# Kernel tuning notes

Measured on AMD Instinct MI355X. Metric: run time of the kernel, lower is better.

Reference implementation:

```python
import jax, jax.numpy as jnp
import numpy as np

D_MODEL = 1024
NUM_HEADS = 16
HEAD_DIM = D_MODEL // NUM_HEADS
SCALE = HEAD_DIM ** -0.5


def setup_inputs() -> dict:
    key = jax.random.key(0)
    ks = jax.random.split(key, 9)
    s = 1.0 / np.sqrt(D_MODEL)
    return {
        "query": jax.random.normal(ks[0], (4, 2048, D_MODEL), dtype=jnp.float32),
        "Wq": jax.random.normal(ks[1], (D_MODEL, D_MODEL), dtype=jnp.float32) * s,
        "bq": jax.random.normal(ks[2], (D_MODEL,), dtype=jnp.float32) * 0.01,
        "Wk": jax.random.normal(ks[3], (D_MODEL, D_MODEL), dtype=jnp.float32) * s,
        "bk": jax.random.normal(ks[4], (D_MODEL,), dtype=jnp.float32) * 0.01,
        "Wv": jax.random.normal(ks[5], (D_MODEL, D_MODEL), dtype=jnp.float32) * s,
        "bv": jax.random.normal(ks[6], (D_MODEL,), dtype=jnp.float32) * 0.01,
        "Wo": jax.random.normal(ks[7], (D_MODEL, D_MODEL), dtype=jnp.float32) * s,
        "bo": jax.random.normal(ks[8], (D_MODEL,), dtype=jnp.float32) * 0.01,
    }


def reference(query, Wq, bq, Wk, bk, Wv, bv, Wo, bo):
    # Self-attention (key=value=query). dropout=0, no mask, so chunked
    # computation equals full softmax attention exactly.
    b, s, d = query.shape
    q = (query @ Wq + bq).reshape(b, s, NUM_HEADS, HEAD_DIM)
    k = (query @ Wk + bk).reshape(b, s, NUM_HEADS, HEAD_DIM)
    v = (query @ Wv + bv).reshape(b, s, NUM_HEADS, HEAD_DIM)
    # scores: [b, h, s_q, s_k]
    scores = jnp.einsum("bqhd,bkhd->bhqk", q, k) * SCALE
    attn = jax.nn.softmax(scores, axis=-1)
    ctx = jnp.einsum("bhqk,bkhd->bqhd", attn, v).reshape(b, s, d)
    return ctx @ Wo + bo
```

## Files before the change

kernel.cpp:

```cpp
#include <hip/hip_runtime.h>
#include <stdint.h>

#define NHEADS 16
#define HDIM   64
#define SEQ    2048
#define BATCH  4
#define DM     1024
#define MTOT   (BATCH*SEQ)
#define SCALE  0.125f
#define QSCALE 0.18033688011112042f

typedef unsigned short u16;
typedef __attribute__((ext_vector_type(8))) short short8;
typedef __attribute__((ext_vector_type(4))) float f32x4;
typedef __attribute__((ext_vector_type(16))) float f32x16;
typedef __attribute__((ext_vector_type(4))) unsigned int u32x4;

__device__ __forceinline__ u16 f2bf(float f) {
  uint32_t u = __builtin_bit_cast(uint32_t, f);
  u += 0x7FFFu + ((u >> 16) & 1u);
  return (u16)(u >> 16);
}

__device__ __forceinline__ f32x4 mfma16(short8 a, short8 b, f32x4 c) {
  return __builtin_amdgcn_mfma_f32_16x16x32_bf16(a, b, c, 0, 0, 0);
}
__device__ __forceinline__ f32x16 mfma32(short8 a, short8 b, f32x16 c) {
  return __builtin_amdgcn_mfma_f32_32x32x16_bf16(a, b, c, 0, 0, 0);
}

__device__ __forceinline__ void gload16(const u16* g, u16* l) {
  __builtin_amdgcn_global_load_lds((const __attribute__((address_space(1))) void*)g,
                                   (__attribute__((address_space(3))) void*)l,
                                   16, 0, 0);
}

#define LDSP(base, row, boff) \
  ((u16*)((char*)(base) + (((row) << 7) + ((boff) ^ (((row) & 7) << 4)))))

__global__ __launch_bounds__(256) void k_conv(const float* __restrict__ in, u16* __restrict__ out) {
  size_t i = (size_t)blockIdx.x * 256 + threadIdx.x;
  const float4* p = (const float4*)(in + i * 8);
  float4 a = p[0], b = p[1];
  u16 r[8] = {f2bf(a.x), f2bf(a.y), f2bf(a.z), f2bf(a.w),
              f2bf(b.x), f2bf(b.y), f2bf(b.z), f2bf(b.w)};
  *(short8*)(out + i * 8) = *(const short8*)r;
}

__global__ __launch_bounds__(256) void k_convw(const float* __restrict__ w0, const float* __restrict__ w1,
                                               const float* __restrict__ w2, const float* __restrict__ w3,
                                               u16* __restrict__ o0, u16* __restrict__ o1,
                                               u16* __restrict__ o2, u16* __restrict__ o3) {
  const float* W = blockIdx.z==0?w0: blockIdx.z==1?w1: blockIdx.z==2?w2:w3;
  u16* O        = blockIdx.z==0?o0: blockIdx.z==1?o1: blockIdx.z==2?o2:o3;
  __shared__ float tile[32][33];
  int t = threadIdx.x;
  int k0 = blockIdx.y*32, n0 = blockIdx.x*32;
  int r = t >> 5, c = t & 31;
  #pragma unroll
  for (int p = 0; p < 4; ++p) tile[r + 8*p][c] = W[(size_t)(k0 + r + 8*p)*DM + n0 + c];
  __syncthreads();
  #pragma unroll
  for (int p = 0; p < 4; ++p) O[(size_t)(n0 + r + 8*p)*DM + k0 + c] = f2bf(tile[c][r + 8*p]);
}

template<int MODE>
__global__ __launch_bounds__(256) void k_gemm(
    const u16* __restrict__ A,
    const u16* __restrict__ WtQ, const u16* __restrict__ WtK, const u16* __restrict__ WtV,
    const float* __restrict__ bQ, const float* __restrict__ bK, const float* __restrict__ bV,
    u16* __restrict__ oQ, u16* __restrict__ oK, u16* __restrict__ oV,
    float* __restrict__ oF)
{
  __shared__ u16 As[128*32];
  __shared__ u16 Bs[128*32];
  const int t = threadIdx.x;
  const int lane = t & 63;
  const int lo = lane & 15, q4 = lane >> 4;
  const int w  = t >> 6, wm = w >> 1, wn = w & 1;

  int m0, n0, z;
  if (MODE == 0) {
    int L = blockIdx.x + 8 * blockIdx.y + 512 * blockIdx.z;
    int work = (L & 7) * 192 + (L >> 3);
    z  = work % 3;
    n0 = ((work / 3) & 7) * 128;
    m0 = (work / 24) * 128;
  } else {
    int L = blockIdx.x + 8 * blockIdx.y;
    int work = (L & 7) * 64 + (L >> 3);
    z  = 0;
    n0 = (work & 7) * 128;
    m0 = (work >> 3) * 128;
  }

  const u16* Wt; const float* bias;
  if (MODE == 0) {
    Wt   = (z==0)?WtQ:(z==1)?WtK:WtV;
    bias = (z==0)?bQ:(z==1)?bK:bV;
  } else { Wt = WtQ; bias = bQ; }

  f32x4 acc[4][4] = {};

  const int gr = lane >> 2;
  const int gc = (lane & 3) * 8;

  for (int kt = 0; kt < 32; ++kt) {
    const int k0 = kt * 32;
    __syncthreads();
    gload16(A  + (size_t)(m0 + w*32 +  0 + gr)*DM + k0 + gc, As + (w*32 +  0)*32);
    gload16(A  + (size_t)(m0 + w*32 + 16 + gr)*DM + k0 + gc, As + (w*32 + 16)*32);
    gload16(Wt + (size_t)(n0 + w*32 +  0 + gr)*DM + k0 + gc, Bs + (w*32 +  0)*32);
    gload16(Wt + (size_t)(n0 + w*32 + 16 + gr)*DM + k0 + gc, Bs + (w*32 + 16)*32);
    __syncthreads();

    short8 af[4], bf[4];
    #pragma unroll
    for (int i = 0; i < 4; ++i)
      af[i] = *(const short8*)(As + (wm*64 + i*16 + lo)*32 + q4*8);
    #pragma unroll
    for (int i = 0; i < 4; ++i)
      bf[i] = *(const short8*)(Bs + (wn*64 + i*16 + lo)*32 + q4*8);
    #pragma unroll
    for (int i = 0; i < 4; ++i)
      #pragma unroll
      for (int j = 0; j < 4; ++j)
        acc[i][j] = mfma16(af[i], bf[j], acc[i][j]);
  }

  #pragma unroll
  for (int i = 0; i < 4; ++i) {
    #pragma unroll
    for (int j = 0; j < 4; ++j) {
      int col = n0 + wn*64 + j*16 + lo;
      float bvv = bias[col];
      #pragma unroll
      for (int r = 0; r < 4; ++r) {
        int row = m0 + wm*64 + i*16 + q4*4 + r;
        float v = acc[i][j][r] + bvv;
        if (MODE == 0) {
          int b = row >> 11, s = row & 2047, h = col >> 6, d = col & 63;
          if (z == 2) oV[(size_t)((b*16 + h)*64 + d)*SEQ + s] = f2bf(v);
          else if (z == 0) oQ[(size_t)((b*16 + h)*SEQ + s)*HDIM + d] = f2bf(v * QSCALE);
          else             oK[(size_t)((b*16 + h)*SEQ + s)*HDIM + d] = f2bf(v);
        } else {
          oF[(size_t)row*DM + col] = v;
        }
      }
    }
  }
}

__global__ __launch_bounds__(256, 2) void k_attn(
    const u16* __restrict__ Q,
    const u16* __restrict__ K,
    const u16* __restrict__ VT,
    u16* __restrict__ O)
{
  __shared__ u16 lds[16384];
  u16* Ks = lds;
  u16* Vs = lds + 4096;
  const int t = threadIdx.x, lane = t & 63, w = t >> 6;
  const int l31 = lane & 31, h = lane >> 5;
  const int bh = blockIdx.x, qt = blockIdx.y;
  const int qw = qt*256 + w*64;

  const u16* Qp = Q  + ((size_t)bh * SEQ + qw) * HDIM;
  const u16* Kp = K  + (size_t)bh * SEQ * HDIM;
  const u16* Vp = VT + (size_t)bh * HDIM * SEQ;

  short8 qf[2][4];
  #pragma unroll
  for (int g = 0; g < 2; ++g)
    #pragma unroll
    for (int c = 0; c < 4; ++c)
      qf[g][c] = *(const short8*)(Qp + (size_t)(g*32 + l31)*HDIM + c*16 + h*8);

  f32x16 acc[2][2] = {};
  float l_run[2] = {0.f, 0.f};

  const int sr = t >> 3, sc = t & 7;
  const u16* Kg = Kp + (size_t)sr * HDIM;
  const u16* Vg = Vp + (size_t)sr * SEQ;
  short8 kr0 = *(const short8*)(Kg + sc*8);
  short8 kr1 = *(const short8*)(Kg + (size_t)32*HDIM + sc*8);
  short8 vr0 = *(const short8*)(Vg + sc*8);
  short8 vr1 = *(const short8*)(Vg + (size_t)32*SEQ + sc*8);

  for (int kt = 0; kt < 32; ++kt) {
    __syncthreads();
    *(short8*)LDSP(Ks, sr,      sc*16) = kr0;
    *(short8*)LDSP(Ks, sr + 32, sc*16) = kr1;
    *(short8*)LDSP(Vs, sr,      sc*16) = vr0;
    *(short8*)LDSP(Vs, sr + 32, sc*16) = vr1;
    {
      int kn = (kt + 1 < 32 ? kt + 1 : 31) * 64;
      kr0 = *(const short8*)(Kg + (size_t)kn*HDIM + sc*8);
      kr1 = *(const short8*)(Kg + (size_t)(kn+32)*HDIM + sc*8);
      vr0 = *(const short8*)(Vg + kn + sc*8);
      vr1 = *(const short8*)(Vg + (size_t)32*SEQ + kn + sc*8);
    }
    __syncthreads();

    #pragma unroll
    for (int kb = 0; kb < 2; ++kb) {
      short8 kf[4];
      #pragma unroll
      for (int c = 0; c < 4; ++c)
        kf[c] = *(const short8*)LDSP(Ks, kb*32 + l31, c*32 + h*16);
      short8 vf[2][2];
      #pragma unroll
      for (int dt = 0; dt < 2; ++dt)
        #pragma unroll
        for (int k2 = 0; k2 < 2; ++k2)
          vf[dt][k2] = *(const short8*)LDSP(Vs, dt*32 + l31, kb*64 + k2*32 + h*16);

      #pragma unroll
      for (int g = 0; g < 2; ++g) {
        f32x16 s = {};
        #pragma unroll
        for (int c = 0; c < 4; ++c) s = mfma32(kf[c], qf[g][c], s);

        float sum = 0.f;
        uint32_t W[8];
        #pragma unroll
        for (int i8 = 0; i8 < 8; ++i8) {
          float pe = exp2f(s[2*i8]);
          float po = exp2f(s[2*i8+1]);
          sum += pe + po;
          W[i8] = __builtin_amdgcn_perm(__builtin_bit_cast(uint32_t, po),
                                        __builtin_bit_cast(uint32_t, pe),
                                        0x07060302u);
        }
        l_run[g] += sum;

        #pragma unroll
        for (int k2 = 0; k2 < 2; ++k2) {
          auto r0 = __builtin_amdgcn_permlane32_swap(W[4*k2 + 0], W[4*k2 + 2], false, false);
          auto r1 = __builtin_amdgcn_permlane32_swap(W[4*k2 + 1], W[4*k2 + 3], false, false);
          u32x4 pw; pw[0] = r0[0]; pw[1] = r1[0]; pw[2] = r0[1]; pw[3] = r1[1];
          short8 pf = __builtin_bit_cast(short8, pw);
          #pragma unroll
          for (int dt = 0; dt < 2; ++dt)
            acc[g][dt] = mfma32(vf[dt][k2], pf, acc[g][dt]);
        }
      }
    }
  }

  __syncthreads();
  u16* ep = lds + w*4096;
  #pragma unroll
  for (int g = 0; g < 2; ++g) {
    float lt = l_run[g] + __shfl_xor(l_run[g], 32);
    float inv = 1.f / lt;
    #pragma unroll
    for (int dt = 0; dt < 2; ++dt)
      #pragma unroll
      for (int i = 0; i < 16; ++i) {
        int d = dt*32 + (i & 3) + 8*(i >> 2) + 4*h;
        *LDSP(ep, g*32 + l31, 2*d) = f2bf(acc[g][dt][i] * inv);
      }
  }
  const int b = bh >> 4, hh = bh & 15;
  #pragma unroll
  for (int it = 0; it < 8; ++it) {
    int row = it*8 + (lane >> 3);
    int s = qw + row;
    short8 v = *(const short8*)LDSP(ep, row, (lane & 7)*16);
    *(short8*)(O + ((size_t)(b*SEQ + s)*NHEADS + hh)*HDIM + (lane & 7)*8) = v;
  }
}

extern "C" void kernel_launch(void* const* d_in, const int* in_sizes, int n_in,
                              void* d_out, int out_size, void* d_ws, size_t ws_size,
                              hipStream_t stream) {
  const float* query = (const float*)d_in[0];
  const float* Wq = (const float*)d_in[1]; const float* bq = (const float*)d_in[2];
  const float* Wk = (const float*)d_in[3]; const float* bk = (const float*)d_in[4];
  const float* Wv = (const float*)d_in[5]; const float* bv = (const float*)d_in[6];
  const float* Wo = (const float*)d_in[7]; const float* bo = (const float*)d_in[8];
  float* out = (float*)d_out;

  u16* qb  = (u16*)d_ws;
  u16* wt0 = qb  + (size_t)MTOT*DM;
  u16* wt1 = wt0 + (size_t)DM*DM;
  u16* wt2 = wt1 + (size_t)DM*DM;
  u16* wt3 = wt2 + (size_t)DM*DM;
  u16* qp  = wt3 + (size_t)DM*DM;
  u16* kp  = qp  + (size_t)MTOT*DM;
  u16* vt  = kp  + (size_t)MTOT*DM;

  k_conv<<<dim3(MTOT*DM/8/256), 256, 0, stream>>>(query, qb);
  k_convw<<<dim3(32, 32, 4), 256, 0, stream>>>(Wq, Wk, Wv, Wo, wt0, wt1, wt2, wt3);
  k_gemm<0><<<dim3(8, 64, 3), 256, 0, stream>>>(qb, wt0, wt1, wt2, bq, bk, bv, qp, kp, vt, nullptr);
  k_attn<<<dim3(64, 8), 256, 0, stream>>>(qp, kp, vt, qb );
  k_gemm<1><<<dim3(8, 64, 1), 256, 0, stream>>>(qb, wt3, nullptr, nullptr, bo, nullptr, nullptr,
                                                nullptr, nullptr, nullptr, out);
}
```

Before: 306.2 us.

## Restructure attention kernel: 8 waves of 32 rows, double-buffered K/V LDS

The attention kernel now launches 512 threads per block, each wave owning 32 query rows instead of 64. K/V tiles are double-buffered in LDS, with one barrier per iteration instead of two, so staging the next tile overlaps compute. It also uses a raw hardware exp2 and packed bf16 epilogue stores. The trade-off is more waves sharing each K/V tile, giving fewer MFMAs per LDS read, plus the approximate exp instruction's precision.

```diff
diff --git a/kernel.cpp b/kernel.cpp
--- a/kernel.cpp
+++ b/kernel.cpp
@@ -20,6 +20,14 @@
   uint32_t u = __builtin_bit_cast(uint32_t, f);
   u += 0x7FFFu + ((u >> 16) & 1u);
   return (u16)(u >> 16);
+}
+
+__device__ __forceinline__ float fexp2(float x) {
+#if __has_builtin(__builtin_amdgcn_exp2f)
+  return __builtin_amdgcn_exp2f(x);
+#else
+  float r; asm("v_exp_f32 %0, %1\n\ts_nop 1" : "=v"(r) : "v"(x)); return r;
+#endif
 }
 
 __device__ __forceinline__ f32x4 mfma16(short8 a, short8 b, f32x4 c) {
@@ -151,120 +159,114 @@
   }
 }
 
-__global__ __launch_bounds__(256, 2) void k_attn(
+__global__ __launch_bounds__(512, 4) void k_attn(
     const u16* __restrict__ Q,
     const u16* __restrict__ K,
     const u16* __restrict__ VT,
     u16* __restrict__ O)
 {
   __shared__ u16 lds[16384];
-  u16* Ks = lds;
-  u16* Vs = lds + 4096;
   const int t = threadIdx.x, lane = t & 63, w = t >> 6;
   const int l31 = lane & 31, h = lane >> 5;
   const int bh = blockIdx.x, qt = blockIdx.y;
-  const int qw = qt*256 + w*64;
+  const int qw = qt*256 + w*32;
 
   const u16* Qp = Q  + ((size_t)bh * SEQ + qw) * HDIM;
   const u16* Kp = K  + (size_t)bh * SEQ * HDIM;
   const u16* Vp = VT + (size_t)bh * HDIM * SEQ;
 
-  short8 qf[2][4];
-  #pragma unroll
-  for (int g = 0; g < 2; ++g)
-    #pragma unroll
-    for (int c = 0; c < 4; ++c)
-      qf[g][c] = *(const short8*)(Qp + (size_t)(g*32 + l31)*HDIM + c*16 + h*8);
-
-  f32x16 acc[2][2] = {};
-  float l_run[2] = {0.f, 0.f};
+  short8 qf[4];
+  #pragma unroll
+  for (int c = 0; c < 4; ++c)
+    qf[c] = *(const short8*)(Qp + (size_t)l31*HDIM + c*16 + h*8);
+
+  f32x16 acc[2] = {};
+  float l_run = 0.f;
 
   const int sr = t >> 3, sc = t & 7;
   const u16* Kg = Kp + (size_t)sr * HDIM;
   const u16* Vg = Vp + (size_t)sr * SEQ;
-  short8 kr0 = *(const short8*)(Kg + sc*8);
-  short8 kr1 = *(const short8*)(Kg + (size_t)32*HDIM + sc*8);
-  short8 vr0 = *(const short8*)(Vg + sc*8);
-  short8 vr1 = *(const short8*)(Vg + (size_t)32*SEQ + sc*8);
+
+  short8 kr = *(const short8*)(Kg + sc*8);
+  short8 vr = *(const short8*)(Vg + sc*8);
+  *(short8*)LDSP(lds,        sr, sc*16) = kr;
+  *(short8*)LDSP(lds + 4096, sr, sc*16) = vr;
+  kr = *(const short8*)(Kg + (size_t)64*HDIM + sc*8);
+  vr = *(const short8*)(Vg + 64 + sc*8);
+  __syncthreads();
 
   for (int kt = 0; kt < 32; ++kt) {
-    __syncthreads();
-    *(short8*)LDSP(Ks, sr,      sc*16) = kr0;
-    *(short8*)LDSP(Ks, sr + 32, sc*16) = kr1;
-    *(short8*)LDSP(Vs, sr,      sc*16) = vr0;
-    *(short8*)LDSP(Vs, sr + 32, sc*16) = vr1;
-    {
-      int kn = (kt + 1 < 32 ? kt + 1 : 31) * 64;
-      kr0 = *(const short8*)(Kg + (size_t)kn*HDIM + sc*8);
-      kr1 = *(const short8*)(Kg + (size_t)(kn+32)*HDIM + sc*8);
-      vr0 = *(const short8*)(Vg + kn + sc*8);
-      vr1 = *(const short8*)(Vg + (size_t)32*SEQ + kn + sc*8);
+    u16* Ksc = lds + (size_t)(kt & 1) * 8192;
+    u16* Vsc = Ksc + 4096;
+    if (kt + 1 < 32) {
+      u16* Ksn = lds + (size_t)((kt + 1) & 1) * 8192;
+      *(short8*)LDSP(Ksn,        sr, sc*16) = kr;
+      *(short8*)LDSP(Ksn + 4096, sr, sc*16) = vr;
+      int kn = (kt + 2 < 32 ? kt + 2 : 31) * 64;
+      kr = *(const short8*)(Kg + (size_t)kn*HDIM + sc*8);
+      vr = *(const short8*)(Vg + kn + sc*8);
     }
-    __syncthreads();
 
     #pragma unroll
     for (int kb = 0; kb < 2; ++kb) {
       short8 kf[4];
       #pragma unroll
       for (int c = 0; c < 4; ++c)
-        kf[c] = *(const short8*)LDSP(Ks, kb*32 + l31, c*32 + h*16);
-      short8 vf[2][2];
-      #pragma unroll
-      for (int dt = 0; dt < 2; ++dt)
+        kf[c] = *(const short8*)LDSP(Ksc, kb*32 + l31, c*32 + h*16);
+
+      f32x16 s = {};
+      #pragma unroll
+      for (int c = 0; c < 4; ++c) s = mfma32(kf[c], qf[c], s);
+
+      float sum = 0.f;
+      uint32_t W[8];
+      #pragma unroll
+      for (int i8 = 0; i8 < 8; ++i8) {
+        float pe = fexp2(s[2*i8]);
+        float po = fexp2(s[2*i8+1]);
+        sum += pe + po;
+        W[i8] = __builtin_amdgcn_perm(__builtin_bit_cast(uint32_t, po),
+                                      __builtin_bit_cast(uint32_t, pe),
+                                      0x07060302u);
+      }
+      l_run += sum;
+
+      #pragma unroll
+      for (int k2 = 0; k2 < 2; ++k2) {
+        auto r0 = __builtin_amdgcn_permlane32_swap(W[4*k2 + 0], W[4*k2 + 2], false, false);
+        auto r1 = __builtin_amdgcn_permlane32_swap(W[4*k2 + 1], W[4*k2 + 3], false, false);
+        u32x4 pw; pw[0] = r0[0]; pw[1] = r1[0]; pw[2] = r0[1]; pw[3] = r1[1];
+        short8 pf = __builtin_bit_cast(short8, pw);
         #pragma unroll
-        for (int k2 = 0; k2 < 2; ++k2)
-          vf[dt][k2] = *(const short8*)LDSP(Vs, dt*32 + l31, kb*64 + k2*32 + h*16);
-
-      #pragma unroll
-      for (int g = 0; g < 2; ++g) {
-        f32x16 s = {};
-        #pragma unroll
-        for (int c = 0; c < 4; ++c) s = mfma32(kf[c], qf[g][c], s);
-
-        float sum = 0.f;
-        uint32_t W[8];
-        #pragma unroll
-        for (int i8 = 0; i8 < 8; ++i8) {
-          float pe = exp2f(s[2*i8]);
-          float po = exp2f(s[2*i8+1]);
-          sum += pe + po;
-          W[i8] = __builtin_amdgcn_perm(__builtin_bit_cast(uint32_t, po),
-                                        __builtin_bit_cast(uint32_t, pe),
-                                        0x07060302u);
-        }
-        l_run[g] += sum;
-
-        #pragma unroll
-        for (int k2 = 0; k2 < 2; ++k2) {
-          auto r0 = __builtin_amdgcn_permlane32_swap(W[4*k2 + 0], W[4*k2 + 2], false, false);
-          auto r1 = __builtin_amdgcn_permlane32_swap(W[4*k2 + 1], W[4*k2 + 3], false, false);
-          u32x4 pw; pw[0] = r0[0]; pw[1] = r1[0]; pw[2] = r0[1]; pw[3] = r1[1];
-          short8 pf = __builtin_bit_cast(short8, pw);
-          #pragma unroll
-          for (int dt = 0; dt < 2; ++dt)
-            acc[g][dt] = mfma32(vf[dt][k2], pf, acc[g][dt]);
+        for (int dt = 0; dt < 2; ++dt) {
+          short8 vf = *(const short8*)LDSP(Vsc, dt*32 + l31, kb*64 + k2*32 + h*16);
+          acc[dt] = mfma32(vf, pf, acc[dt]);
         }
       }
     }
-  }
-
-  __syncthreads();
-  u16* ep = lds + w*4096;
-  #pragma unroll
-  for (int g = 0; g < 2; ++g) {
-    float lt = l_run[g] + __shfl_xor(l_run[g], 32);
-    float inv = 1.f / lt;
-    #pragma unroll
-    for (int dt = 0; dt < 2; ++dt)
-      #pragma unroll
-      for (int i = 0; i < 16; ++i) {
-        int d = dt*32 + (i & 3) + 8*(i >> 2) + 4*h;
-        *LDSP(ep, g*32 + l31, 2*d) = f2bf(acc[g][dt][i] * inv);
-      }
-  }
+    __syncthreads();
+  }
+
+  u16* ep = lds + w*2048;
+  float lt = l_run + __shfl_xor(l_run, 32);
+  float inv = 1.f / lt;
+  #pragma unroll
+  for (int dt = 0; dt < 2; ++dt)
+    #pragma unroll
+    for (int grp = 0; grp < 4; ++grp) {
+      int dbase = dt*32 + 8*grp + 4*h;
+      uint32_t w0 = __builtin_amdgcn_perm(
+          __builtin_bit_cast(uint32_t, acc[dt][grp*4+1] * inv),
+          __builtin_bit_cast(uint32_t, acc[dt][grp*4+0] * inv), 0x07060302u);
+      uint32_t w1 = __builtin_amdgcn_perm(
+          __builtin_bit_cast(uint32_t, acc[dt][grp*4+3] * inv),
+          __builtin_bit_cast(uint32_t, acc[dt][grp*4+2] * inv), 0x07060302u);
+      uint2 pk; pk.x = w0; pk.y = w1;
+      *(uint2*)LDSP(ep, l31, 2*dbase) = pk;
+    }
   const int b = bh >> 4, hh = bh & 15;
   #pragma unroll
-  for (int it = 0; it < 8; ++it) {
+  for (int it = 0; it < 4; ++it) {
     int row = it*8 + (lane >> 3);
     int s = qw + row;
     short8 v = *(const short8*)LDSP(ep, row, (lane & 7)*16);
@@ -294,7 +296,7 @@
   k_conv<<<dim3(MTOT*DM/8/256), 256, 0, stream>>>(query, qb);
   k_convw<<<dim3(32, 32, 4), 256, 0, stream>>>(Wq, Wk, Wv, Wo, wt0, wt1, wt2, wt3);
   k_gemm<0><<<dim3(8, 64, 3), 256, 0, stream>>>(qb, wt0, wt1, wt2, bq, bk, bv, qp, kp, vt, nullptr);
-  k_attn<<<dim3(64, 8), 256, 0, stream>>>(qp, kp, vt, qb );
+  k_attn<<<dim3(64, 8), 512, 0, stream>>>(qp, kp, vt, qb );
   k_gemm<1><<<dim3(8, 64, 1), 256, 0, stream>>>(qb, wt3, nullptr, nullptr, bo, nullptr, nullptr,
                                                 nullptr, nullptr, nullptr, out);
 }
```

Result: faster. 288.2 us (-5.9%).
